# Kernel optimization log

Hardware: AMD Instinct MI355X
Metric: run time of the kernel (lower is better)

Reference implementation:

```python
import jax, jax.numpy as jnp
import numpy as np

H = 768
NH = 12
HD = H // NH
FF = 3072
EPS = 1e-5
CHUNK = 32  # query chunk for L1 distance to bound memory


def layer_norm(x, g, b):
    mu = jnp.mean(x, axis=-1, keepdims=True)
    var = jnp.mean((x - mu) ** 2, axis=-1, keepdims=True)
    return (x - mu) / jnp.sqrt(var + EPS) * g + b


def l1_distance(Q, K):
    # Q, K: [BH, S, D] -> [BH, S, S], computed in query chunks to avoid
    # materializing the full [BH, S, S, D] broadcast intermediate.
    BH, S, D = Q.shape
    nc = S // CHUNK
    Qc = Q.reshape(BH, nc, CHUNK, D).transpose(1, 0, 2, 3)  # [nc, BH, c, D]

    def f(qc):  # qc: [BH, c, D]
        return jnp.sum(jnp.abs(qc[:, :, None, :] - K[:, None, :, :]), axis=-1)

    d = jax.lax.map(f, Qc)  # [nc, BH, c, S]
    return d.transpose(1, 0, 2, 3).reshape(BH, S, S)


def setup_inputs() -> dict:
    key = jax.random.key(0)
    ks = jax.random.split(key, 12)
    sd = 0.02
    B, S = 2, 1024
    return {
        'hidden_states': jax.random.normal(ks[0], (B, S, H), jnp.float32),
        'ln1_g': jnp.ones((H,), jnp.float32),
        'ln1_b': jnp.zeros((H,), jnp.float32),
        'Wq': jax.random.normal(ks[1], (H, H), jnp.float32) * sd,
        'bq': jnp.zeros((H,), jnp.float32),
        'Wk': jax.random.normal(ks[2], (H, H), jnp.float32) * sd,
        'bk': jnp.zeros((H,), jnp.float32),
        'Wv': jax.random.normal(ks[3], (H, H), jnp.float32) * sd,
        'bv': jnp.zeros((H,), jnp.float32),
        'Wo': jax.random.normal(ks[4], (H, H), jnp.float32) * sd,
        'bo': jnp.zeros((H,), jnp.float32),
        'lam': jnp.asarray(1.0, jnp.float32),
        'ln2_g': jnp.ones((H,), jnp.float32),
        'ln2_b': jnp.zeros((H,), jnp.float32),
        'W1': jax.random.normal(ks[5], (H, FF), jnp.float32) * sd,
        'b1': jnp.zeros((FF,), jnp.float32),
        'W2': jax.random.normal(ks[6], (FF, H), jnp.float32) * sd,
        'b2': jnp.zeros((H,), jnp.float32),
    }


def reference(hidden_states, ln1_g, ln1_b, Wq, bq, Wk, bk, Wv, bv, Wo, bo,
              lam, ln2_g, ln2_b, W1, b1, W2, b2):
    B, S, _ = hidden_states.shape
    scale = 1.0 / np.sqrt(HD)

    residual = hidden_states
    x = layer_norm(hidden_states, ln1_g, ln1_b)

    Q = (x @ Wq + bq).reshape(B, S, NH, HD).transpose(0, 2, 1, 3)  # [B,H,S,D]
    K = (x @ Wk + bk).reshape(B, S, NH, HD).transpose(0, 2, 1, 3)
    V = (x @ Wv + bv).reshape(B, S, NH, HD).transpose(0, 2, 1, 3)

    Qf = Q.reshape(B * NH, S, HD)
    Kf = K.reshape(B * NH, S, HD)
    dist = l1_distance(Qf, Kf).reshape(B, NH, S, S)

    scores = -lam * dist * scale
    attn = jax.nn.softmax(scores, axis=-1)  # [B,H,S,S]

    out = jnp.einsum('bhqk,bhkd->bhqd', attn, V)
    out = out.transpose(0, 2, 1, 3).reshape(B, S, H)
    out = out @ Wo + bo
    out = residual + out

    residual = out
    y = layer_norm(out, ln2_g, ln2_b)
    y = jax.nn.gelu(y @ W1 + b1, approximate=False) @ W2 + b2
    out = residual + y
    return out, attn
```

## Files before the change

### kernel.cpp

```cpp
#include <hip/hip_runtime.h>
#include <cstdint>
#include <cstddef>

#define SB    1024
#define BB    2
#define HH    768
#define NHH   12
#define HDD   64
#define FFF   3072
#define RR    (BB*SB)
#define NQKV  2304

#define QSCALE 42.5f

typedef __attribute__((ext_vector_type(8))) short short8;
typedef __attribute__((ext_vector_type(4))) float f4;

__device__ __forceinline__ unsigned short f2bf(float f) {
  union { float f; unsigned u; } x; x.f = f;
  unsigned r = x.u + 0x7FFFu + ((x.u >> 16) & 1u);
  return (unsigned short)(r >> 16);
}

__device__ __forceinline__ unsigned qz8(float x) {
  int v = (int)rintf(x * QSCALE) + 128;
  v = v < 0 ? 0 : (v > 255 ? 255 : v);
  return (unsigned)v;
}

__device__ __forceinline__ void async16(void* lds, const void* g) {
  __builtin_amdgcn_global_load_lds((const __attribute__((address_space(1))) unsigned int*)g,
                                   (__attribute__((address_space(3))) unsigned int*)lds,
                                   16, 0, 0);
}

__global__ __launch_bounds__(256)
void prep_all(const float* __restrict__ Wq, const float* __restrict__ Wk,
              const float* __restrict__ Wv, const float* __restrict__ Wo,
              const float* __restrict__ W1, const float* __restrict__ W2,
              const float* __restrict__ bq, const float* __restrict__ bk,
              const float* __restrict__ bv,
              const float* __restrict__ hidden, const float* __restrict__ ln1_g,
              const float* __restrict__ ln1_b,
              unsigned short* __restrict__ Wqkv_t, unsigned short* __restrict__ W1t,
              unsigned short* __restrict__ W2t, float* __restrict__ bqkv,
              unsigned short* __restrict__ xb) {
  const int t = blockIdx.x;
  const int tid = threadIdx.x;
  __shared__ float tile[64][65];
  __shared__ float rs[4], rq[4];
  if (t >= 1737) {
    const int row = t - 1737;
    const float* x = hidden + (size_t)row * HH;
    float v0 = x[tid], v1 = x[tid + 256], v2 = x[tid + 512];
    float s = v0 + v1 + v2;
    float q = v0 * v0 + v1 * v1 + v2 * v2;
    #pragma unroll
    for (int o = 32; o >= 1; o >>= 1) { s += __shfl_xor(s, o); q += __shfl_xor(q, o); }
    const int w = tid >> 6;
    if ((tid & 63) == 0) { rs[w] = s; rq[w] = q; }
    __syncthreads();
    s = rs[0] + rs[1] + rs[2] + rs[3];
    q = rq[0] + rq[1] + rq[2] + rq[3];
    float mean = s * (1.0f / HH);
    float rstd = rsqrtf(q * (1.0f / HH) - mean * mean + 1e-5f);
    unsigned short* o0 = xb + (size_t)row * HH;
    o0[tid]       = f2bf((v0 - mean) * rstd * ln1_g[tid]       + ln1_b[tid]);
    o0[tid + 256] = f2bf((v1 - mean) * rstd * ln1_g[tid + 256] + ln1_b[tid + 256]);
    o0[tid + 512] = f2bf((v2 - mean) * rstd * ln1_g[tid + 512] + ln1_b[tid + 512]);
    return;
  }
  if (t >= 1728) {
    int i = (t - 1728) * 256 + tid;
    if (i < NQKV)
      bqkv[i] = (i < HH) ? bq[i] : (i < 2 * HH ? bk[i - HH] : bv[i - 2 * HH]);
    return;
  }
  const float* in; unsigned short* out; int ldin, ldout, r0, c0;
  if (t < 576) {
    int m = t / 144, q = t % 144;
    in = m == 0 ? Wq : (m == 1 ? Wk : (m == 2 ? Wv : Wo));
    out = Wqkv_t + (size_t)m * HH * HH;
    ldin = HH; ldout = HH;
    r0 = (q / 12) * 64; c0 = (q % 12) * 64;
  } else if (t < 1152) {
    int q = t - 576;
    in = W1; out = W1t; ldin = FFF; ldout = HH;
    r0 = (q % 12) * 64; c0 = (q / 12) * 64;
  } else {
    int q = t - 1152;
    in = W2; out = W2t; ldin = HH; ldout = FFF;
    r0 = (q % 48) * 64; c0 = (q / 48) * 64;
  }
  for (int i = tid; i < 4096; i += 256) {
    int r = i >> 6, c = i & 63;
    tile[r][c] = in[(size_t)(r0 + r) * ldin + c0 + c];
  }
  __syncthreads();
  for (int i = tid; i < 4096; i += 256) {
    int cc = i >> 6, rr = i & 63;
    out[(size_t)(c0 + cc) * ldout + r0 + rr] = f2bf(tile[rr][cc]);
  }
}

__global__ __launch_bounds__(256)
void gemm_qkv(const unsigned short* __restrict__ A, const unsigned short* __restrict__ Bt,
              const float* __restrict__ bqkv, unsigned* __restrict__ Qq,
              unsigned* __restrict__ Kq, unsigned short* __restrict__ Vt) {
  __shared__ __align__(16) unsigned char smem[49152];
  unsigned short (*lA)[128 * 32] = (unsigned short (*)[128 * 32])smem;
  unsigned short (*lB)[128 * 32] = (unsigned short (*)[128 * 32])(smem + 24576);
  const unsigned short* Ab = A + (size_t)blockIdx.y * 128 * HH;
  const unsigned short* Bb = Bt + (size_t)blockIdx.x * 128 * HH;
  const int tid = threadIdx.x;
  const int wave = tid >> 6, lane = tid & 63;
  const int wr = wave >> 1, wc = wave & 1;
  const int lo = lane & 15, hi = lane >> 4;

  auto stage = [&](int k0, int buf) {
    #pragma unroll
    for (int i = 0; i < 512; i += 256) {
      int idx = i + tid; int r = idx >> 2, kg = idx & 3;
      async16(&lA[buf][idx * 8], &Ab[(size_t)r * HH + k0 + kg * 8]);
    }
    #pragma unroll
    for (int i = 0; i < 512; i += 256) {
      int idx = i + tid; int r = idx >> 2, kg = idx & 3;
      async16(&lB[buf][idx * 8], &Bb[(size_t)r * HH + k0 + kg * 8]);
    }
  };

  stage(0, 0);
  stage(32, 1);
  f4 acc[4][4] = {};
  for (int it = 0; it < 24; it++) {
    if (it + 1 < 24) {
      asm volatile("s_waitcnt vmcnt(4)" ::: "memory");
    } else {
      asm volatile("s_waitcnt vmcnt(0)" ::: "memory");
    }
    __builtin_amdgcn_s_barrier();
    __builtin_amdgcn_sched_barrier(0);
    const int cur = it % 3;
    short8 af[4], bf[4];
    #pragma unroll
    for (int i = 0; i < 4; i++)
      af[i] = *(const short8*)&lA[cur][(wr * 64 + i * 16 + lo) * 32 + hi * 8];
    #pragma unroll
    for (int j = 0; j < 4; j++)
      bf[j] = *(const short8*)&lB[cur][(wc * 64 + j * 16 + lo) * 32 + hi * 8];
    if (it + 2 < 24) stage((it + 2) * 32, (it + 2) % 3);
    #pragma unroll
    for (int i = 0; i < 4; i++)
      #pragma unroll
      for (int j = 0; j < 4; j++)
        acc[i][j] = __builtin_amdgcn_mfma_f32_16x16x32_bf16(af[i], bf[j], acc[i][j], 0, 0, 0);
  }
  __syncthreads();

  const int reg = blockIdx.x / 6;
  const int cb = blockIdx.x * 128;
  if (reg < 2) {
    unsigned char* t8 = smem;
    #pragma unroll
    for (int i = 0; i < 4; i++)
      #pragma unroll
      for (int j = 0; j < 4; j++) {
        int col = wc * 64 + j * 16 + lo;
        float bv_ = bqkv[cb + col];
        #pragma unroll
        for (int r = 0; r < 4; r++) {
          int row = wr * 64 + i * 16 + hi * 4 + r;
          t8[row * 132 + col] = (unsigned char)qz8(acc[i][j][r] + bv_);
        }
      }
    __syncthreads();
    const unsigned* t32 = (const unsigned*)smem;
    if (reg == 0) {
      #pragma unroll
      for (int i0 = 0; i0 < 4096; i0 += 256) {
        int idx = i0 + tid;
        int cw = idx & 31, rw = idx >> 5;
        int token = blockIdx.y * 128 + rw;
        Qq[(size_t)token * 192 + blockIdx.x * 32 + cw] = t32[rw * 33 + cw];
      }
    } else {
      #pragma unroll
      for (int i0 = 0; i0 < 4096; i0 += 256) {
        int idx = i0 + tid;
        int rw = idx & 127, cw = idx >> 7;
        int token = blockIdx.y * 128 + rw;
        int b = token >> 10, k = token & 1023;
        int dgG = (blockIdx.x - 6) * 32 + cw;
        Kq[(size_t)((b * NHH + (dgG >> 4)) * 16 + (dgG & 15)) * SB + k] = t32[rw * 33 + cw];
      }
    }
  } else {
    unsigned short* t16 = (unsigned short*)smem;
    #pragma unroll
    for (int i = 0; i < 4; i++)
      #pragma unroll
      for (int j = 0; j < 4; j++) {
        int col = wc * 64 + j * 16 + lo;
        float bv_ = bqkv[cb + col];
        #pragma unroll
        for (int r = 0; r < 4; r++) {
          int row = wr * 64 + i * 16 + hi * 4 + r;
          t16[col * 130 + row] = f2bf(acc[i][j][r] + bv_);
        }
      }
    __syncthreads();
    const unsigned* tv = (const unsigned*)smem;
    unsigned* VtU = (unsigned*)Vt;
    #pragma unroll
    for (int i0 = 0; i0 < 8192; i0 += 256) {
      int idx = i0 + tid;
      int rp = idx & 63, cw = idx >> 6;
      int gcol = (blockIdx.x - 12) * 128 + cw;
      int h = gcol >> 6, d = gcol & 63;
      int b = blockIdx.y >> 3;
      VtU[(size_t)((b * NHH + h) * HDD + d) * 512 + (blockIdx.y & 7) * 64 + rp] =
          tv[cw * 65 + rp];
    }
  }
}

template<int BM, int BN, int WR, int WC, int MODE, int KS>
__global__ __launch_bounds__(WR*WC*64)
void gemm_bt(const unsigned short* __restrict__ A, int ldA,
             const unsigned short* __restrict__ Bt, int ldB,
             void* __restrict__ Cv, int ldC,
             const float* __restrict__ bias,
             int K, long partStride) {
  constexpr int T = WR * WC * 64;
  constexpr int LPT = (BM * 4 + BN * 4) / T;
  __shared__ unsigned short lA[3][BM * 32];
  __shared__ unsigned short lB[3][BN * 32];
  const int ks = blockIdx.z;
  const int KH = K / KS;
  const unsigned short* Ab = A + (size_t)blockIdx.y * BM * ldA + (size_t)ks * KH;
  const unsigned short* Bb = Bt + (size_t)blockIdx.x * BN * ldB + (size_t)ks * KH;
  const long cOff = (long)blockIdx.y * BM * ldC + (long)blockIdx.x * BN
                  + (long)ks * partStride;
  const int tid = threadIdx.x;
  const int wave = tid >> 6, lane = tid & 63;
  const int wr = wave / WC, wc = wave % WC;
  const int lo = lane & 15, hi = lane >> 4;

  auto stage = [&](int k0, int buf) {
    #pragma unroll
    for (int i = 0; i < BM * 4; i += T) {
      int idx = i + tid; int r = idx >> 2, kg = idx & 3;
      async16(&lA[buf][idx * 8], &Ab[(size_t)r * ldA + k0 + kg * 8]);
    }
    #pragma unroll
    for (int i = 0; i < BN * 4; i += T) {
      int idx = i + tid; int r = idx >> 2, kg = idx & 3;
      async16(&lB[buf][idx * 8], &Bb[(size_t)r * ldB + k0 + kg * 8]);
    }
  };

  const int nIter = KH / 32;
  stage(0, 0);
  if (nIter > 1) stage(32, 1);
  f4 acc[4][4] = {};
  for (int it = 0; it < nIter; it++) {
    if (it + 1 < nIter) {
      asm volatile("s_waitcnt vmcnt(%0)" :: "n"(LPT) : "memory");
    } else {
      asm volatile("s_waitcnt vmcnt(0)" ::: "memory");
    }
    __builtin_amdgcn_s_barrier();
    __builtin_amdgcn_sched_barrier(0);
    const int cur = it % 3;
    short8 af[4], bf[4];
    #pragma unroll
    for (int i = 0; i < 4; i++)
      af[i] = *(const short8*)&lA[cur][(wr * 64 + i * 16 + lo) * 32 + hi * 8];
    #pragma unroll
    for (int j = 0; j < 4; j++)
      bf[j] = *(const short8*)&lB[cur][(wc * 64 + j * 16 + lo) * 32 + hi * 8];
    if (it + 2 < nIter) stage((it + 2) * 32, (it + 2) % 3);
    #pragma unroll
    for (int i = 0; i < 4; i++)
      #pragma unroll
      for (int j = 0; j < 4; j++)
        acc[i][j] = __builtin_amdgcn_mfma_f32_16x16x32_bf16(af[i], bf[j], acc[i][j], 0, 0, 0);
  }
  float* Cf = (float*)Cv;
  unsigned short* Cb = (unsigned short*)Cv;
  const int bc0 = blockIdx.x * BN;
  #pragma unroll
  for (int i = 0; i < 4; i++) {
    #pragma unroll
    for (int j = 0; j < 4; j++) {
      int col = wc * 64 + j * 16 + lo;
      #pragma unroll
      for (int r = 0; r < 4; r++) {
        int row = wr * 64 + i * 16 + hi * 4 + r;
        size_t idx = (size_t)cOff + (size_t)row * ldC + col;
        float v = acc[i][j][r];
        if constexpr (MODE == 3) {
          float tt = v + bias[bc0 + col];
          Cb[idx] = f2bf(0.5f * tt * (1.0f + erff(tt * 0.70710678118654752f)));
        } else {
          Cf[idx] = v;
        }
      }
    }
  }
}

__global__ __launch_bounds__(256)
void reduce_ln(const float* __restrict__ p, const float* __restrict__ bias,
               const float* __restrict__ res, const float* __restrict__ g,
               const float* __restrict__ bb, float* __restrict__ attnOut,
               unsigned short* __restrict__ out) {
  const int row = blockIdx.x, tid = threadIdx.x;
  const size_t rb = (size_t)row * HH;
  float v[3]; float s = 0.f, q = 0.f;
  #pragma unroll
  for (int j = 0; j < 3; j++) {
    int c = tid + j * 256;
    size_t idx = rb + c;
    float a = p[idx] + p[(size_t)RR * HH + idx] + p[2 * (size_t)RR * HH + idx]
            + p[3 * (size_t)RR * HH + idx] + bias[c] + res[idx];
    attnOut[idx] = a;
    v[j] = a; s += a; q += a * a;
  }
  #pragma unroll
  for (int o = 32; o >= 1; o >>= 1) { s += __shfl_xor(s, o); q += __shfl_xor(q, o); }
  __shared__ float rs[4], rq[4];
  const int w = tid >> 6;
  if ((tid & 63) == 0) { rs[w] = s; rq[w] = q; }
  __syncthreads();
  s = rs[0] + rs[1] + rs[2] + rs[3];
  q = rq[0] + rq[1] + rq[2] + rq[3];
  float mean = s * (1.0f / HH);
  float rstd = rsqrtf(q * (1.0f / HH) - mean * mean + 1e-5f);
  #pragma unroll
  for (int j = 0; j < 3; j++) {
    int c = tid + j * 256;
    out[rb + c] = f2bf((v[j] - mean) * rstd * g[c] + bb[c]);
  }
}

__global__ __launch_bounds__(256)
void reduce4_bias_res(const float* __restrict__ p, const float* __restrict__ bias,
                      const float* __restrict__ res, float* __restrict__ out) {
  int i = (blockIdx.x * 256 + threadIdx.x) * 4;
  int col = i % HH;
  float4 a = *(const float4*)(p + i);
  #pragma unroll
  for (int s = 1; s < 4; s++) {
    float4 b = *(const float4*)(p + (size_t)s * RR * HH + i);
    a.x += b.x; a.y += b.y; a.z += b.z; a.w += b.w;
  }
  float4 bb = *(const float4*)(bias + col);
  float4 r = *(const float4*)(res + i);
  float4 o;
  o.x = a.x + bb.x + r.x;
  o.y = a.y + bb.y + r.y;
  o.z = a.z + bb.z + r.z;
  o.w = a.w + bb.w + r.w;
  *(float4*)(out + i) = o;
}

#define DQ 16
__global__ __launch_bounds__(512)
void dist_softmax_pv(const unsigned* __restrict__ Qq, const unsigned* __restrict__ Kq,
                     const unsigned short* __restrict__ Vt,
                     const float* __restrict__ lam_p,
                     float* __restrict__ attnF, unsigned short* __restrict__ ctx) {
  __shared__ __align__(16) unsigned lk[8 * SB];
  __shared__ unsigned lq[DQ * 16];
  const int bh = blockIdx.y;
  const int q0 = blockIdx.x * DQ;
  const int b = bh / NHH, h = bh % NHH;
  const int tid = threadIdx.x;
  const int w = tid >> 6, lane = tid & 63;
  const int lo = lane & 15, hi = lane >> 4;

  if (tid < 256) {
    int r = tid >> 4, dg = tid & 15;
    lq[r * 16 + dg] = Qq[(size_t)(b * SB + q0 + r) * 192 + h * 16 + dg];
  }

  const unsigned* Ks = Kq + (size_t)bh * 16 * SB;
  unsigned acc[2][4][4] = {};
  const unsigned* lqw = &lq[(w * 2) * 16];

  #pragma unroll
  for (int ch = 0; ch < 2; ch++) {
    #pragma unroll
    for (int i = 0; i < 4; i++)
      async16(&lk[(i * 512 + tid) * 4], Ks + (size_t)ch * 8192 + (i * 512 + tid) * 4);
    __syncthreads();
    #pragma unroll
    for (int dg = 0; dg < 8; dg++) {
      unsigned qd[2];
      #pragma unroll
      for (int qi = 0; qi < 2; qi++) qd[qi] = lqw[qi * 16 + ch * 8 + dg];
      uint4 kv[4];
      #pragma unroll
      for (int kg = 0; kg < 4; kg++)
        kv[kg] = *(const uint4*)&lk[dg * SB + kg * 256 + lane * 4];
      #pragma unroll
      for (int qi = 0; qi < 2; qi++) {
        #pragma unroll
        for (int kg = 0; kg < 4; kg++) {
          acc[qi][kg][0] = __builtin_amdgcn_sad_u8(qd[qi], kv[kg].x, acc[qi][kg][0]);
          acc[qi][kg][1] = __builtin_amdgcn_sad_u8(qd[qi], kv[kg].y, acc[qi][kg][1]);
          acc[qi][kg][2] = __builtin_amdgcn_sad_u8(qd[qi], kv[kg].z, acc[qi][kg][2]);
          acc[qi][kg][3] = __builtin_amdgcn_sad_u8(qd[qi], kv[kg].w, acc[qi][kg][3]);
        }
      }
    }
    __syncthreads();
  }

  unsigned short* lp = (unsigned short*)lk;
  const float kscl = -lam_p[0] * 0.125f / QSCALE;
  #pragma unroll
  for (int qi = 0; qi < 2; qi++) {
    float sc[16];
    float m = -1e30f;
    #pragma unroll
    for (int kg = 0; kg < 4; kg++)
      #pragma unroll
      for (int c = 0; c < 4; c++) {
        float v = (float)acc[qi][kg][c] * kscl;
        sc[kg * 4 + c] = v;
        m = fmaxf(m, v);
      }
    #pragma unroll
    for (int off = 1; off < 64; off <<= 1) m = fmaxf(m, __shfl_xor(m, off));
    float s = 0.f;
    #pragma unroll
    for (int i = 0; i < 16; i++) {
      float e = __expf(sc[i] - m);
      sc[i] = e;
      s += e;
    }
    #pragma unroll
    for (int off = 1; off < 64; off <<= 1) s += __shfl_xor(s, off);
    const float rinv = 1.0f / s;
    const int row = w * 2 + qi;
    const size_t gb = (size_t)bh * SB * SB + (size_t)(q0 + row) * SB + lane * 4;
    #pragma unroll
    for (int kg = 0; kg < 4; kg++) {
      float4 p;
      p.x = sc[kg * 4 + 0] * rinv;
      p.y = sc[kg * 4 + 1] * rinv;
      p.z = sc[kg * 4 + 2] * rinv;
      p.w = sc[kg * 4 + 3] * rinv;
      *(float4*)&attnF[gb + kg * 256] = p;
      ushort4 pb;
      pb.x = f2bf(p.x); pb.y = f2bf(p.y); pb.z = f2bf(p.z); pb.w = f2bf(p.w);
      *(ushort4*)&lp[row * SB + kg * 256 + lane * 4] = pb;
    }
  }
  __syncthreads();

  if (w < 4) {
    const unsigned short* Vb = Vt + ((size_t)bh * HDD + w * 16 + lo) * SB + hi * 8;
    const unsigned short* Pb = lp + lo * SB + hi * 8;
    f4 cacc = {0.f, 0.f, 0.f, 0.f};
    #pragma unroll
    for (int k0 = 0; k0 < SB; k0 += 32) {
      short8 af = *(const short8*)(Pb + k0);
      short8 bf = *(const short8*)(Vb + k0);
      cacc = __builtin_amdgcn_mfma_f32_16x16x32_bf16(af, bf, cacc, 0, 0, 0);
    }
    unsigned short* cb = ctx + (size_t)(b * SB + q0 + hi * 4) * HH + h * HDD + w * 16 + lo;
    #pragma unroll
    for (int r = 0; r < 4; r++) cb[(size_t)r * HH] = f2bf(cacc[r]);
  }
}

extern "C" void kernel_launch(void* const* d_in, const int* in_sizes, int n_in,
                              void* d_out, int out_size, void* d_ws, size_t ws_size,
                              hipStream_t stream) {
  (void)in_sizes; (void)n_in; (void)out_size; (void)ws_size;
  const float* hidden = (const float*)d_in[0];
  const float* ln1_g  = (const float*)d_in[1];
  const float* ln1_b  = (const float*)d_in[2];
  const float* Wq     = (const float*)d_in[3];
  const float* bq     = (const float*)d_in[4];
  const float* Wk     = (const float*)d_in[5];
  const float* bk     = (const float*)d_in[6];
  const float* Wv     = (const float*)d_in[7];
  const float* bv     = (const float*)d_in[8];
  const float* Wo     = (const float*)d_in[9];
  const float* bo     = (const float*)d_in[10];
  const float* lam    = (const float*)d_in[11];
  const float* ln2_g  = (const float*)d_in[12];
  const float* ln2_b  = (const float*)d_in[13];
  const float* W1     = (const float*)d_in[14];
  const float* b1     = (const float*)d_in[15];
  const float* W2     = (const float*)d_in[16];
  const float* b2     = (const float*)d_in[17];

  float* out0  = (float*)d_out;
  float* attnF = out0 + (size_t)RR * HH;

  char* w = (char*)d_ws;
  auto alloc = [&](size_t bytes) { char* p = w; w += (bytes + 255) & ~(size_t)255; return p; };
  unsigned short* xb      = (unsigned short*)alloc((size_t)RR * HH * 2);
  unsigned short* Wqkv_t  = (unsigned short*)alloc((size_t)NQKV * HH * 2);
  unsigned short* Wo_t    = (unsigned short*)alloc((size_t)HH * HH * 2);
  unsigned short* W1t     = (unsigned short*)alloc((size_t)FFF * HH * 2);
  unsigned short* W2t     = (unsigned short*)alloc((size_t)HH * FFF * 2);
  float*          bqkv    = (float*)alloc((size_t)NQKV * 4);
  unsigned*       Qq      = (unsigned*)alloc((size_t)RR * 192 * 4);
  unsigned*       Kq      = (unsigned*)alloc((size_t)BB * NHH * 16 * SB * 4);
  unsigned short* Vt      = (unsigned short*)alloc((size_t)BB * NHH * HDD * SB * 2);
  unsigned short* ctx     = (unsigned short*)alloc((size_t)RR * HH * 2);
  float*          attnOut = (float*)alloc((size_t)RR * HH * 4);
  unsigned short* h1      = (unsigned short*)alloc((size_t)RR * FFF * 2);
  float*          gPart   = (float*)alloc((size_t)4 * RR * HH * 4);
  unsigned short* y2      = Vt;
  (void)Wo_t;

  prep_all<<<dim3(1737 + RR), 256, 0, stream>>>(Wq, Wk, Wv, Wo, W1, W2, bq, bk, bv,
                                                hidden, ln1_g, ln1_b,
                                                Wqkv_t, W1t, W2t, bqkv, xb);

  gemm_qkv<<<dim3(NQKV / 128, RR / 128), 256, 0, stream>>>(
      xb, Wqkv_t, bqkv, Qq, Kq, Vt);

  dist_softmax_pv<<<dim3(SB / DQ, BB * NHH), 512, 0, stream>>>(
      Qq, Kq, Vt, lam, attnF, ctx);

  gemm_bt<128, 128, 2, 2, 4, 4><<<dim3(HH / 128, RR / 128, 4), 256, 0, stream>>>(
      ctx, HH, Wqkv_t + (size_t)3 * HH * HH, HH, gPart, HH,
      nullptr, HH, (long)RR * HH);

  reduce_ln<<<dim3(RR), 256, 0, stream>>>(gPart, bo, hidden, ln2_g, ln2_b,
                                          attnOut, y2);

  gemm_bt<128, 128, 2, 2, 3, 1><<<dim3(FFF / 128, RR / 128, 1), 256, 0, stream>>>(
      y2, HH, W1t, HH, h1, FFF, b1, HH, 0);

  gemm_bt<128, 128, 2, 2, 4, 4><<<dim3(HH / 128, RR / 128, 4), 256, 0, stream>>>(
      h1, FFF, W2t, FFF, gPart, HH, nullptr, FFF, (long)RR * HH);

  reduce4_bias_res<<<dim3(RR * HH / 1024), 256, 0, stream>>>(gPart, b2, attnOut, out0);
}
```

Before: 283.5 us.

## Shrink distance kernel to 256 threads, swizzle P in LDS, use nontemporal memory ops

The fused distance/softmax/PV kernel now runs 256 threads per block, and each wave handles 4 query rows instead of 2. This reuses each K load from LDS across more SAD operations. All four waves now take part in the PV MFMA, and the bf16 probability tile in LDS gets an XOR swizzle to cut bank conflicts on the MFMA operand reads. Separately, the split-K partial buffers and the large attention-probability output use nontemporal stores and loads to keep streaming data from polluting cache. The trade-offs are higher register pressure in the distance kernel and fewer threads to hide latency.

```diff
diff --git a/kernel.cpp b/kernel.cpp
--- a/kernel.cpp
+++ b/kernel.cpp
@@ -304,7 +304,7 @@
           float tt = v + bias[bc0 + col];
           Cb[idx] = f2bf(0.5f * tt * (1.0f + erff(tt * 0.70710678118654752f)));
         } else {
-          Cf[idx] = v;
+          __builtin_nontemporal_store(v, &Cf[idx]);
         }
       }
     }
@@ -323,8 +323,11 @@
   for (int j = 0; j < 3; j++) {
     int c = tid + j * 256;
     size_t idx = rb + c;
-    float a = p[idx] + p[(size_t)RR * HH + idx] + p[2 * (size_t)RR * HH + idx]
-            + p[3 * (size_t)RR * HH + idx] + bias[c] + res[idx];
+    float a = __builtin_nontemporal_load(&p[idx])
+            + __builtin_nontemporal_load(&p[(size_t)RR * HH + idx])
+            + __builtin_nontemporal_load(&p[2 * (size_t)RR * HH + idx])
+            + __builtin_nontemporal_load(&p[3 * (size_t)RR * HH + idx])
+            + bias[c] + res[idx];
     attnOut[idx] = a;
     v[j] = a; s += a; q += a * a;
   }
@@ -350,14 +353,14 @@
                       const float* __restrict__ res, float* __restrict__ out) {
   int i = (blockIdx.x * 256 + threadIdx.x) * 4;
   int col = i % HH;
-  float4 a = *(const float4*)(p + i);
+  f4 a = __builtin_nontemporal_load((const f4*)(p + i));
   #pragma unroll
   for (int s = 1; s < 4; s++) {
-    float4 b = *(const float4*)(p + (size_t)s * RR * HH + i);
-    a.x += b.x; a.y += b.y; a.z += b.z; a.w += b.w;
-  }
-  float4 bb = *(const float4*)(bias + col);
-  float4 r = *(const float4*)(res + i);
+    f4 b = __builtin_nontemporal_load((const f4*)(p + (size_t)s * RR * HH + i));
+    a += b;
+  }
+  const float4 bb = *(const float4*)(bias + col);
+  const float4 r = *(const float4*)(res + i);
   float4 o;
   o.x = a.x + bb.x + r.x;
   o.y = a.y + bb.y + r.y;
@@ -367,7 +370,7 @@
 }
 
 #define DQ 16
-__global__ __launch_bounds__(512)
+__global__ __launch_bounds__(256)
 void dist_softmax_pv(const unsigned* __restrict__ Qq, const unsigned* __restrict__ Kq,
                      const unsigned short* __restrict__ Vt,
                      const float* __restrict__ lam_p,
@@ -381,32 +384,32 @@
   const int w = tid >> 6, lane = tid & 63;
   const int lo = lane & 15, hi = lane >> 4;
 
-  if (tid < 256) {
+  {
     int r = tid >> 4, dg = tid & 15;
     lq[r * 16 + dg] = Qq[(size_t)(b * SB + q0 + r) * 192 + h * 16 + dg];
   }
 
   const unsigned* Ks = Kq + (size_t)bh * 16 * SB;
-  unsigned acc[2][4][4] = {};
-  const unsigned* lqw = &lq[(w * 2) * 16];
+  unsigned acc[4][4][4] = {};
+  const unsigned* lqw = &lq[(w * 4) * 16];
 
   #pragma unroll
   for (int ch = 0; ch < 2; ch++) {
     #pragma unroll
-    for (int i = 0; i < 4; i++)
-      async16(&lk[(i * 512 + tid) * 4], Ks + (size_t)ch * 8192 + (i * 512 + tid) * 4);
+    for (int i = 0; i < 8; i++)
+      async16(&lk[(i * 256 + tid) * 4], Ks + (size_t)ch * 8192 + (i * 256 + tid) * 4);
     __syncthreads();
     #pragma unroll
     for (int dg = 0; dg < 8; dg++) {
-      unsigned qd[2];
-      #pragma unroll
-      for (int qi = 0; qi < 2; qi++) qd[qi] = lqw[qi * 16 + ch * 8 + dg];
+      unsigned qd[4];
+      #pragma unroll
+      for (int qi = 0; qi < 4; qi++) qd[qi] = lqw[qi * 16 + ch * 8 + dg];
       uint4 kv[4];
       #pragma unroll
       for (int kg = 0; kg < 4; kg++)
         kv[kg] = *(const uint4*)&lk[dg * SB + kg * 256 + lane * 4];
       #pragma unroll
-      for (int qi = 0; qi < 2; qi++) {
+      for (int qi = 0; qi < 4; qi++) {
         #pragma unroll
         for (int kg = 0; kg < 4; kg++) {
           acc[qi][kg][0] = __builtin_amdgcn_sad_u8(qd[qi], kv[kg].x, acc[qi][kg][0]);
@@ -422,7 +425,7 @@
   unsigned short* lp = (unsigned short*)lk;
   const float kscl = -lam_p[0] * 0.125f / QSCALE;
   #pragma unroll
-  for (int qi = 0; qi < 2; qi++) {
+  for (int qi = 0; qi < 4; qi++) {
     float sc[16];
     float m = -1e30f;
     #pragma unroll
@@ -445,30 +448,32 @@
     #pragma unroll
     for (int off = 1; off < 64; off <<= 1) s += __shfl_xor(s, off);
     const float rinv = 1.0f / s;
-    const int row = w * 2 + qi;
+    const int row = w * 4 + qi;
+    const unsigned swz = (unsigned)((row & 7) << 3);
     const size_t gb = (size_t)bh * SB * SB + (size_t)(q0 + row) * SB + lane * 4;
     #pragma unroll
     for (int kg = 0; kg < 4; kg++) {
-      float4 p;
+      f4 p;
       p.x = sc[kg * 4 + 0] * rinv;
       p.y = sc[kg * 4 + 1] * rinv;
       p.z = sc[kg * 4 + 2] * rinv;
       p.w = sc[kg * 4 + 3] * rinv;
-      *(float4*)&attnF[gb + kg * 256] = p;
+      __builtin_nontemporal_store(p, (f4*)&attnF[gb + kg * 256]);
       ushort4 pb;
       pb.x = f2bf(p.x); pb.y = f2bf(p.y); pb.z = f2bf(p.z); pb.w = f2bf(p.w);
-      *(ushort4*)&lp[row * SB + kg * 256 + lane * 4] = pb;
+      *(ushort4*)&lp[(unsigned)(row * SB + kg * 256 + lane * 4) ^ swz] = pb;
     }
   }
   __syncthreads();
 
-  if (w < 4) {
+  {
     const unsigned short* Vb = Vt + ((size_t)bh * HDD + w * 16 + lo) * SB + hi * 8;
-    const unsigned short* Pb = lp + lo * SB + hi * 8;
+    const unsigned pswz = (unsigned)((lo & 7) << 3);
+    const unsigned pbase = (unsigned)(lo * SB + hi * 8);
     f4 cacc = {0.f, 0.f, 0.f, 0.f};
     #pragma unroll
     for (int k0 = 0; k0 < SB; k0 += 32) {
-      short8 af = *(const short8*)(Pb + k0);
+      short8 af = *(const short8*)&lp[(pbase + k0) ^ pswz];
       short8 bf = *(const short8*)(Vb + k0);
       cacc = __builtin_amdgcn_mfma_f32_16x16x32_bf16(af, bf, cacc, 0, 0, 0);
     }
@@ -529,7 +534,7 @@
   gemm_qkv<<<dim3(NQKV / 128, RR / 128), 256, 0, stream>>>(
       xb, Wqkv_t, bqkv, Qq, Kq, Vt);
 
-  dist_softmax_pv<<<dim3(SB / DQ, BB * NHH), 512, 0, stream>>>(
+  dist_softmax_pv<<<dim3(SB / DQ, BB * NHH), 256, 0, stream>>>(
       Qq, Kq, Vt, lam, attnF, ctx);
 
   gemm_bt<128, 128, 2, 2, 4, 4><<<dim3(HH / 128, RR / 128, 4), 256, 0, stream>>>(
```

After: 281.6 us. No clear change (-0.7%).
